# Performance work log

Measured on AMD Instinct MI355X. Metric: run time of the kernel, lower is better.

Reference implementation:

```python
import jax, jax.numpy as jnp
import numpy as np

N_NODES = 50000
N_EDGES = 1600000
N_HEAD = 4
F_OUT = 128


def setup_inputs() -> dict:
    key = jax.random.key(0)
    k1, k2, k3, k4 = jax.random.split(key, 4)
    x = jax.random.normal(k1, (N_NODES, F_OUT), dtype=jnp.float32)
    # diag weight [H,1,F]; small scale like xavier on a diag-ish param
    w = jax.random.normal(k2, (N_HEAD, 1, F_OUT), dtype=jnp.float32) * 0.1
    # a_src_dst init: uniform(-stdv, stdv), stdv = 1/sqrt(2*f_out)
    stdv = 1.0 / np.sqrt(2 * F_OUT)
    a = jax.random.uniform(k3, (N_HEAD, 2 * F_OUT, 1), dtype=jnp.float32, minval=-stdv, maxval=stdv)
    edge_index = jax.random.randint(k4, (2, N_EDGES), 0, N_NODES, dtype=jnp.int64)
    return {"x": x, "w": w, "a": a, "edge_index": edge_index}


def reference(x, w, a, edge_index):
    # x: [N,F], w: [H,1,F] (diag), a: [H,2F,1], edge_index: [2,E]
    H, F = w.shape[0], w.shape[-1]
    N = x.shape[0]
    src = edge_index[0]  # row indices (aggregation targets)
    dst = edge_index[1]
    h = x[None, :, :] * w  # [H,N,F]  (diag: elementwise scale per head)
    # split cat(h_src,h_dst)@a into two per-node projections (same math as concat+matmul)
    a_src = a[:, :F, 0]  # [H,F]
    a_dst = a[:, F:, 0]  # [H,F]
    s_src = jnp.einsum('hnf,hf->hn', h, a_src)  # [H,N]
    s_dst = jnp.einsum('hnf,hf->hn', h, a_dst)  # [H,N]
    score = s_src[:, src] + s_dst[:, dst]  # [H,E]
    edge_e = jnp.exp(-jax.nn.leaky_relu(score, negative_slope=0.2))  # [H,E]
    outs = []
    for i in range(H):  # small fixed head loop keeps peak memory at one head's messages
        rowsum = jax.ops.segment_sum(edge_e[i], src, num_segments=N)  # [N]
        msg = edge_e[i][:, None] * h[i][dst]  # [E,F]
        agg = jax.ops.segment_sum(msg, src, num_segments=N)  # [N,F]
        outs.append(agg / rowsum[:, None])
    return jnp.stack(outs, axis=0)  # [H,N,F]
```

## Files before the change

### kernel.cpp

```cpp
#include <hip/hip_runtime.h>

#define N_NODES 50000
#define N_EDGES 1600000
#define N_HEAD 4
#define F_OUT 128
#define CAP 96
#define NPS 512
#define K1 98
#define SCAP 17408
#define NPG 32
#define GROUPS 1563
#define EPB 4096
#define P1_BLOCKS ((N_EDGES + EPB - 1) / EPB)

__global__ void __launch_bounds__(256) score_kernel(
    const float* __restrict__ x, const float* __restrict__ w,
    const float* __restrict__ a, float4* __restrict__ s_src4,
    float4* __restrict__ s_dst4) {
  int wv = (blockIdx.x * blockDim.x + threadIdx.x) >> 6;
  int lane = threadIdx.x & 63;
  if (wv >= N_NODES) return;
  float xv0 = x[wv * F_OUT + lane];
  float xv1 = x[wv * F_OUT + 64 + lane];
  float ps[N_HEAD], pd[N_HEAD];
#pragma unroll
  for (int h = 0; h < N_HEAD; ++h) {
    float w0 = w[h * F_OUT + lane];
    float w1 = w[h * F_OUT + 64 + lane];
    float as0 = a[h * 2 * F_OUT + lane];
    float as1 = a[h * 2 * F_OUT + 64 + lane];
    float ad0 = a[h * 2 * F_OUT + F_OUT + lane];
    float ad1 = a[h * 2 * F_OUT + F_OUT + 64 + lane];
    ps[h] = xv0 * w0 * as0 + xv1 * w1 * as1;
    pd[h] = xv0 * w0 * ad0 + xv1 * w1 * ad1;
  }
#pragma unroll
  for (int off = 32; off > 0; off >>= 1) {
#pragma unroll
    for (int h = 0; h < N_HEAD; ++h) {
      ps[h] += __shfl_xor(ps[h], off, 64);
      pd[h] += __shfl_xor(pd[h], off, 64);
    }
  }
  if (lane == 0) {
    s_src4[wv] = make_float4(ps[0], ps[1], ps[2], ps[3]);
    s_dst4[wv] = make_float4(pd[0], pd[1], pd[2], pd[3]);
  }
}

__global__ void __launch_bounds__(256) partition_kernel(
    const int* __restrict__ src, const int* __restrict__ dst,
    int* __restrict__ gc, unsigned int* __restrict__ region) {
  __shared__ int hist[K1], cur[K1], lstart[K1], gpos[K1];
  __shared__ unsigned int staging[EPB];
  const int tid = threadIdx.x;
  const int base = blockIdx.x * EPB;
  int vc = N_EDGES - base;
  if (vc > EPB) vc = EPB;

  unsigned int pk[EPB / 256];
#pragma unroll
  for (int k = 0; k < EPB / 256; ++k) {
    int i = k * 256 + tid;
    if (i < vc) {
      unsigned int s = (unsigned int)src[base + i];
      unsigned int d = (unsigned int)dst[base + i];
      pk[k] = (s << 16) | d;
    } else {
      pk[k] = 0xffffffffu;
    }
  }
  if (tid < K1) { hist[tid] = 0; cur[tid] = 0; }
  __syncthreads();
#pragma unroll
  for (int k = 0; k < EPB / 256; ++k)
    if (pk[k] != 0xffffffffu) atomicAdd(&hist[pk[k] >> 25], 1);
  __syncthreads();
  if (tid < 64) {
    int carry = 0;
    for (int b0 = 0; b0 < K1; b0 += 64) {
      int idx = b0 + tid;
      int h = (idx < K1) ? hist[idx] : 0;
      int v = h;
#pragma unroll
      for (int off = 1; off < 64; off <<= 1) {
        int t = __shfl_up(v, off, 64);
        if (tid >= off) v += t;
      }
      if (idx < K1) {
        lstart[idx] = carry + v - h;
        gpos[idx] = atomicAdd(&gc[idx], h);
      }
      carry += __shfl(v, 63, 64);
    }
  }
  __syncthreads();
#pragma unroll
  for (int k = 0; k < EPB / 256; ++k) {
    if (pk[k] != 0xffffffffu) {
      int b = pk[k] >> 25;
      int pos = lstart[b] + atomicAdd(&cur[b], 1);
      staging[pos] = pk[k];
    }
  }
  __syncthreads();
  for (int i = tid; i < vc; i += 256) {
    unsigned int v = staging[i];
    int b = v >> 25;
    int off = gpos[b] + (i - lstart[b]);
    if (off < SCAP) region[(size_t)b * SCAP + off] = v;
  }
}

__global__ void __launch_bounds__(256) agg_kernel(
    const float* __restrict__ x, const float* __restrict__ w,
    const float4* __restrict__ s_src4, const float4* __restrict__ s_dst4,
    const int* __restrict__ gc, const unsigned int* __restrict__ region,
    float* __restrict__ out) {
  __shared__ int ncnt[NPG];
  __shared__ int nbkt[NPG][CAP];
  __shared__ float4 lds_w[4][CAP];
  const int tid = threadIdx.x;
  const int g = blockIdx.x;
  const int sb = g >> 4;
  int c = gc[sb];
  if (c > SCAP) c = SCAP;
  if (tid < NPG) ncnt[tid] = 0;
  __syncthreads();

  const unsigned int* reg = region + (size_t)sb * SCAP;
  const unsigned int gtag = (unsigned int)g;
  for (int i = tid; i < c; i += 256) {
    unsigned int v = reg[i];
    unsigned int s = v >> 16;
    if ((s >> 5) == gtag) {
      int l = s & 31;
      int p = atomicAdd(&ncnt[l], 1);
      if (p < CAP) nbkt[l][p] = (int)(v & 0xffffu);
    }
  }
  __syncthreads();

  const int ws = tid >> 6, lane = tid & 63;
  const float* xp = x + 2 * lane;

  for (int l = ws; l < NPG; l += 4) {
    int n = g * NPG + l;
    if (n >= N_NODES) break;
    int m = ncnt[l];
    m = (m < CAP) ? m : CAP;
    float4 ss = s_src4[n];

    float p0 = 0.f, p1 = 0.f, p2 = 0.f, p3 = 0.f;
    for (int j = lane; j < m; j += 64) {
      int d = nbkt[l][j];
      float4 sd = s_dst4[d];
      float sc0 = ss.x + sd.x, sc1 = ss.y + sd.y, sc2 = ss.z + sd.z, sc3 = ss.w + sd.w;
      float e0 = __expf(-fmaxf(sc0, 0.2f * sc0));
      float e1 = __expf(-fmaxf(sc1, 0.2f * sc1));
      float e2 = __expf(-fmaxf(sc2, 0.2f * sc2));
      float e3 = __expf(-fmaxf(sc3, 0.2f * sc3));
      lds_w[ws][j] = make_float4(e0, e1, e2, e3);
      p0 += e0; p1 += e1; p2 += e2; p3 += e3;
    }
#pragma unroll
    for (int off = 32; off > 0; off >>= 1) {
      p0 += __shfl_xor(p0, off, 64);
      p1 += __shfl_xor(p1, off, 64);
      p2 += __shfl_xor(p2, off, 64);
      p3 += __shfl_xor(p3, off, 64);
    }

    float2 a0 = {0.f, 0.f}, a1 = {0.f, 0.f}, a2 = {0.f, 0.f}, a3 = {0.f, 0.f};
    int j = 0;
    for (; j + 1 < m; j += 2) {
      int d0 = nbkt[l][j];
      int d1 = nbkt[l][j + 1];
      float4 w0 = lds_w[ws][j];
      float4 w1 = lds_w[ws][j + 1];
      float2 x0 = *(const float2*)(xp + (size_t)d0 * F_OUT);
      float2 x1 = *(const float2*)(xp + (size_t)d1 * F_OUT);
      a0.x = fmaf(w0.x, x0.x, a0.x); a0.y = fmaf(w0.x, x0.y, a0.y);
      a1.x = fmaf(w0.y, x0.x, a1.x); a1.y = fmaf(w0.y, x0.y, a1.y);
      a2.x = fmaf(w0.z, x0.x, a2.x); a2.y = fmaf(w0.z, x0.y, a2.y);
      a3.x = fmaf(w0.w, x0.x, a3.x); a3.y = fmaf(w0.w, x0.y, a3.y);
      a0.x = fmaf(w1.x, x1.x, a0.x); a0.y = fmaf(w1.x, x1.y, a0.y);
      a1.x = fmaf(w1.y, x1.x, a1.x); a1.y = fmaf(w1.y, x1.y, a1.y);
      a2.x = fmaf(w1.z, x1.x, a2.x); a2.y = fmaf(w1.z, x1.y, a2.y);
      a3.x = fmaf(w1.w, x1.x, a3.x); a3.y = fmaf(w1.w, x1.y, a3.y);
    }
    if (j < m) {
      int d0 = nbkt[l][j];
      float4 w0 = lds_w[ws][j];
      float2 x0 = *(const float2*)(xp + (size_t)d0 * F_OUT);
      a0.x = fmaf(w0.x, x0.x, a0.x); a0.y = fmaf(w0.x, x0.y, a0.y);
      a1.x = fmaf(w0.y, x0.x, a1.x); a1.y = fmaf(w0.y, x0.y, a1.y);
      a2.x = fmaf(w0.z, x0.x, a2.x); a2.y = fmaf(w0.z, x0.y, a2.y);
      a3.x = fmaf(w0.w, x0.x, a3.x); a3.y = fmaf(w0.w, x0.y, a3.y);
    }

    const float2 wl0 = *(const float2*)(w + 0 * F_OUT + 2 * lane);
    const float2 wl1 = *(const float2*)(w + 1 * F_OUT + 2 * lane);
    const float2 wl2 = *(const float2*)(w + 2 * F_OUT + 2 * lane);
    const float2 wl3 = *(const float2*)(w + 3 * F_OUT + 2 * lane);
    float r0 = 1.f / p0, r1 = 1.f / p1, r2 = 1.f / p2, r3 = 1.f / p3;

    float2 o;
    o.x = wl0.x * a0.x * r0; o.y = wl0.y * a0.y * r0;
    *(float2*)(out + ((size_t)0 * N_NODES + n) * F_OUT + 2 * lane) = o;
    o.x = wl1.x * a1.x * r1; o.y = wl1.y * a1.y * r1;
    *(float2*)(out + ((size_t)1 * N_NODES + n) * F_OUT + 2 * lane) = o;
    o.x = wl2.x * a2.x * r2; o.y = wl2.y * a2.y * r2;
    *(float2*)(out + ((size_t)2 * N_NODES + n) * F_OUT + 2 * lane) = o;
    o.x = wl3.x * a3.x * r3; o.y = wl3.y * a3.y * r3;
    *(float2*)(out + ((size_t)3 * N_NODES + n) * F_OUT + 2 * lane) = o;
  }
}

extern "C" void kernel_launch(void* const* d_in, const int* in_sizes, int n_in,
                              void* d_out, int out_size, void* d_ws, size_t ws_size,
                              hipStream_t stream) {
  const float* x = (const float*)d_in[0];
  const float* w = (const float*)d_in[1];
  const float* a = (const float*)d_in[2];
  const int* ei = (const int*)d_in[3];
  const int* src = ei;
  const int* dst = ei + N_EDGES;
  float* out = (float*)d_out;

  char* p = (char*)d_ws;
  float4* s_src4 = (float4*)p;      p += (size_t)N_NODES * 16;
  float4* s_dst4 = (float4*)p;      p += (size_t)N_NODES * 16;
  int* gc = (int*)p;                p += 4096;
  unsigned int* region = (unsigned int*)p;
  p += (size_t)K1 * SCAP * 4;

  hipMemsetAsync(gc, 0, 4096, stream);

  score_kernel<<<(N_NODES * 64 + 255) / 256, 256, 0, stream>>>(x, w, a, s_src4, s_dst4);
  partition_kernel<<<P1_BLOCKS, 256, 0, stream>>>(src, dst, gc, region);
  agg_kernel<<<GROUPS, 256, 0, stream>>>(x, w, s_src4, s_dst4, gc, region, out);
}
```

Baseline: 308.9 us.

## Use float4 half-wave gathers, smaller node groups, and fold memset into score kernel

```diff
diff --git a/kernel.cpp b/kernel.cpp
--- a/kernel.cpp
+++ b/kernel.cpp
@@ -8,15 +8,16 @@
 #define NPS 512
 #define K1 98
 #define SCAP 17408
-#define NPG 32
-#define GROUPS 1563
-#define EPB 4096
+#define NPG 16
+#define GROUPS 3125
+#define EPB 2048
 #define P1_BLOCKS ((N_EDGES + EPB - 1) / EPB)
 
 __global__ void __launch_bounds__(256) score_kernel(
     const float* __restrict__ x, const float* __restrict__ w,
     const float* __restrict__ a, float4* __restrict__ s_src4,
-    float4* __restrict__ s_dst4) {
+    float4* __restrict__ s_dst4, int* __restrict__ gc) {
+  if (blockIdx.x == 0 && threadIdx.x < K1) gc[threadIdx.x] = 0;
   int wv = (blockIdx.x * blockDim.x + threadIdx.x) >> 6;
   int lane = threadIdx.x & 63;
   if (wv >= N_NODES) return;
@@ -112,7 +113,7 @@
   }
 }
 
-__global__ void __launch_bounds__(256) agg_kernel(
+__global__ void __launch_bounds__(256, 8) agg_kernel(
     const float* __restrict__ x, const float* __restrict__ w,
     const float4* __restrict__ s_src4, const float4* __restrict__ s_dst4,
     const int* __restrict__ gc, const unsigned int* __restrict__ region,
@@ -122,7 +123,7 @@
   __shared__ float4 lds_w[4][CAP];
   const int tid = threadIdx.x;
   const int g = blockIdx.x;
-  const int sb = g >> 4;
+  const int sb = g >> 5;
   int c = gc[sb];
   if (c > SCAP) c = SCAP;
   if (tid < NPG) ncnt[tid] = 0;
@@ -133,8 +134,8 @@
   for (int i = tid; i < c; i += 256) {
     unsigned int v = reg[i];
     unsigned int s = v >> 16;
-    if ((s >> 5) == gtag) {
-      int l = s & 31;
+    if ((s >> 4) == gtag) {
+      int l = s & 15;
       int p = atomicAdd(&ncnt[l], 1);
       if (p < CAP) nbkt[l][p] = (int)(v & 0xffffu);
     }
@@ -142,7 +143,9 @@
   __syncthreads();
 
   const int ws = tid >> 6, lane = tid & 63;
-  const float* xp = x + 2 * lane;
+  const int half = lane >> 5, fl = lane & 31;
+  const float4* __restrict__ xq = (const float4*)x;
+  const float4* __restrict__ wq = (const float4*)w;
 
   for (int l = ws; l < NPG; l += 4) {
     int n = g * NPG + l;
@@ -171,49 +174,88 @@
       p3 += __shfl_xor(p3, off, 64);
     }
 
-    float2 a0 = {0.f, 0.f}, a1 = {0.f, 0.f}, a2 = {0.f, 0.f}, a3 = {0.f, 0.f};
+    float4 A0 = {0, 0, 0, 0}, A1 = {0, 0, 0, 0}, A2 = {0, 0, 0, 0}, A3 = {0, 0, 0, 0};
     int j = 0;
+    for (; j + 3 < m; j += 4) {
+      int da = nbkt[l][j + half];
+      int db = nbkt[l][j + 2 + half];
+      float4 wa = lds_w[ws][j + half];
+      float4 wb = lds_w[ws][j + 2 + half];
+      float4 xa = xq[(size_t)da * 32 + fl];
+      float4 xb = xq[(size_t)db * 32 + fl];
+      A0.x = fmaf(wa.x, xa.x, A0.x); A0.y = fmaf(wa.x, xa.y, A0.y);
+      A0.z = fmaf(wa.x, xa.z, A0.z); A0.w = fmaf(wa.x, xa.w, A0.w);
+      A1.x = fmaf(wa.y, xa.x, A1.x); A1.y = fmaf(wa.y, xa.y, A1.y);
+      A1.z = fmaf(wa.y, xa.z, A1.z); A1.w = fmaf(wa.y, xa.w, A1.w);
+      A2.x = fmaf(wa.z, xa.x, A2.x); A2.y = fmaf(wa.z, xa.y, A2.y);
+      A2.z = fmaf(wa.z, xa.z, A2.z); A2.w = fmaf(wa.z, xa.w, A2.w);
+      A3.x = fmaf(wa.w, xa.x, A3.x); A3.y = fmaf(wa.w, xa.y, A3.y);
+      A3.z = fmaf(wa.w, xa.z, A3.z); A3.w = fmaf(wa.w, xa.w, A3.w);
+      A0.x = fmaf(wb.x, xb.x, A0.x); A0.y = fmaf(wb.x, xb.y, A0.y);
+      A0.z = fmaf(wb.x, xb.z, A0.z); A0.w = fmaf(wb.x, xb.w, A0.w);
+      A1.x = fmaf(wb.y, xb.x, A1.x); A1.y = fmaf(wb.y, xb.y, A1.y);
+      A1.z = fmaf(wb.y, xb.z, A1.z); A1.w = fmaf(wb.y, xb.w, A1.w);
+      A2.x = fmaf(wb.z, xb.x, A2.x); A2.y = fmaf(wb.z, xb.y, A2.y);
+      A2.z = fmaf(wb.z, xb.z, A2.z); A2.w = fmaf(wb.z, xb.w, A2.w);
+      A3.x = fmaf(wb.w, xb.x, A3.x); A3.y = fmaf(wb.w, xb.y, A3.y);
+      A3.z = fmaf(wb.w, xb.z, A3.z); A3.w = fmaf(wb.w, xb.w, A3.w);
+    }
     for (; j + 1 < m; j += 2) {
-      int d0 = nbkt[l][j];
-      int d1 = nbkt[l][j + 1];
-      float4 w0 = lds_w[ws][j];
-      float4 w1 = lds_w[ws][j + 1];
-      float2 x0 = *(const float2*)(xp + (size_t)d0 * F_OUT);
-      float2 x1 = *(const float2*)(xp + (size_t)d1 * F_OUT);
-      a0.x = fmaf(w0.x, x0.x, a0.x); a0.y = fmaf(w0.x, x0.y, a0.y);
-      a1.x = fmaf(w0.y, x0.x, a1.x); a1.y = fmaf(w0.y, x0.y, a1.y);
-      a2.x = fmaf(w0.z, x0.x, a2.x); a2.y = fmaf(w0.z, x0.y, a2.y);
-      a3.x = fmaf(w0.w, x0.x, a3.x); a3.y = fmaf(w0.w, x0.y, a3.y);
-      a0.x = fmaf(w1.x, x1.x, a0.x); a0.y = fmaf(w1.x, x1.y, a0.y);
-      a1.x = fmaf(w1.y, x1.x, a1.x); a1.y = fmaf(w1.y, x1.y, a1.y);
-      a2.x = fmaf(w1.z, x1.x, a2.x); a2.y = fmaf(w1.z, x1.y, a2.y);
-      a3.x = fmaf(w1.w, x1.x, a3.x); a3.y = fmaf(w1.w, x1.y, a3.y);
+      int da = nbkt[l][j + half];
+      float4 wa = lds_w[ws][j + half];
+      float4 xa = xq[(size_t)da * 32 + fl];
+      A0.x = fmaf(wa.x, xa.x, A0.x); A0.y = fmaf(wa.x, xa.y, A0.y);
+      A0.z = fmaf(wa.x, xa.z, A0.z); A0.w = fmaf(wa.x, xa.w, A0.w);
+      A1.x = fmaf(wa.y, xa.x, A1.x); A1.y = fmaf(wa.y, xa.y, A1.y);
+      A1.z = fmaf(wa.y, xa.z, A1.z); A1.w = fmaf(wa.y, xa.w, A1.w);
+      A2.x = fmaf(wa.z, xa.x, A2.x); A2.y = fmaf(wa.z, xa.y, A2.y);
+      A2.z = fmaf(wa.z, xa.z, A2.z); A2.w = fmaf(wa.z, xa.w, A2.w);
+      A3.x = fmaf(wa.w, xa.x, A3.x); A3.y = fmaf(wa.w, xa.y, A3.y);
+      A3.z = fmaf(wa.w, xa.z, A3.z); A3.w = fmaf(wa.w, xa.w, A3.w);
     }
     if (j < m) {
-      int d0 = nbkt[l][j];
-      float4 w0 = lds_w[ws][j];
-      float2 x0 = *(const float2*)(xp + (size_t)d0 * F_OUT);
-      a0.x = fmaf(w0.x, x0.x, a0.x); a0.y = fmaf(w0.x, x0.y, a0.y);
-      a1.x = fmaf(w0.y, x0.x, a1.x); a1.y = fmaf(w0.y, x0.y, a1.y);
-      a2.x = fmaf(w0.z, x0.x, a2.x); a2.y = fmaf(w0.z, x0.y, a2.y);
-      a3.x = fmaf(w0.w, x0.x, a3.x); a3.y = fmaf(w0.w, x0.y, a3.y);
-    }
-
-    const float2 wl0 = *(const float2*)(w + 0 * F_OUT + 2 * lane);
-    const float2 wl1 = *(const float2*)(w + 1 * F_OUT + 2 * lane);
-    const float2 wl2 = *(const float2*)(w + 2 * F_OUT + 2 * lane);
-    const float2 wl3 = *(const float2*)(w + 3 * F_OUT + 2 * lane);
+      int da = nbkt[l][j];
+      float4 wa = lds_w[ws][j];
+      float4 xa = xq[(size_t)da * 32 + fl];
+      if (half == 0) {
+        A0.x = fmaf(wa.x, xa.x, A0.x); A0.y = fmaf(wa.x, xa.y, A0.y);
+        A0.z = fmaf(wa.x, xa.z, A0.z); A0.w = fmaf(wa.x, xa.w, A0.w);
+        A1.x = fmaf(wa.y, xa.x, A1.x); A1.y = fmaf(wa.y, xa.y, A1.y);
+        A1.z = fmaf(wa.y, xa.z, A1.z); A1.w = fmaf(wa.y, xa.w, A1.w);
+        A2.x = fmaf(wa.z, xa.x, A2.x); A2.y = fmaf(wa.z, xa.y, A2.y);
+        A2.z = fmaf(wa.z, xa.z, A2.z); A2.w = fmaf(wa.z, xa.w, A2.w);
+        A3.x = fmaf(wa.w, xa.x, A3.x); A3.y = fmaf(wa.w, xa.y, A3.y);
+        A3.z = fmaf(wa.w, xa.z, A3.z); A3.w = fmaf(wa.w, xa.w, A3.w);
+      }
+    }
+
+    A0.x += __shfl_xor(A0.x, 32, 64); A0.y += __shfl_xor(A0.y, 32, 64);
+    A0.z += __shfl_xor(A0.z, 32, 64); A0.w += __shfl_xor(A0.w, 32, 64);
+    A1.x += __shfl_xor(A1.x, 32, 64); A1.y += __shfl_xor(A1.y, 32, 64);
+    A1.z += __shfl_xor(A1.z, 32, 64); A1.w += __shfl_xor(A1.w, 32, 64);
+    A2.x += __shfl_xor(A2.x, 32, 64); A2.y += __shfl_xor(A2.y, 32, 64);
+    A2.z += __shfl_xor(A2.z, 32, 64); A2.w += __shfl_xor(A2.w, 32, 64);
+    A3.x += __shfl_xor(A3.x, 32, 64); A3.y += __shfl_xor(A3.y, 32, 64);
+    A3.z += __shfl_xor(A3.z, 32, 64); A3.w += __shfl_xor(A3.w, 32, 64);
+
     float r0 = 1.f / p0, r1 = 1.f / p1, r2 = 1.f / p2, r3 = 1.f / p3;
 
-    float2 o;
-    o.x = wl0.x * a0.x * r0; o.y = wl0.y * a0.y * r0;
-    *(float2*)(out + ((size_t)0 * N_NODES + n) * F_OUT + 2 * lane) = o;
-    o.x = wl1.x * a1.x * r1; o.y = wl1.y * a1.y * r1;
-    *(float2*)(out + ((size_t)1 * N_NODES + n) * F_OUT + 2 * lane) = o;
-    o.x = wl2.x * a2.x * r2; o.y = wl2.y * a2.y * r2;
-    *(float2*)(out + ((size_t)2 * N_NODES + n) * F_OUT + 2 * lane) = o;
-    o.x = wl3.x * a3.x * r3; o.y = wl3.y * a3.y * r3;
-    *(float2*)(out + ((size_t)3 * N_NODES + n) * F_OUT + 2 * lane) = o;
+    {
+      float4 acc; float rr; int h;
+      if (half == 0) { acc = A0; rr = r0; h = 0; } else { acc = A1; rr = r1; h = 1; }
+      float4 ww = wq[h * 32 + fl];
+      float4 o = {ww.x * acc.x * rr, ww.y * acc.y * rr,
+                  ww.z * acc.z * rr, ww.w * acc.w * rr};
+      ((float4*)out)[((size_t)h * N_NODES + n) * 32 + fl] = o;
+    }
+    {
+      float4 acc; float rr; int h;
+      if (half == 0) { acc = A2; rr = r2; h = 2; } else { acc = A3; rr = r3; h = 3; }
+      float4 ww = wq[h * 32 + fl];
+      float4 o = {ww.x * acc.x * rr, ww.y * acc.y * rr,
+                  ww.z * acc.z * rr, ww.w * acc.w * rr};
+      ((float4*)out)[((size_t)h * N_NODES + n) * 32 + fl] = o;
+    }
   }
 }
 
@@ -235,9 +277,7 @@
   unsigned int* region = (unsigned int*)p;
   p += (size_t)K1 * SCAP * 4;
 
-  hipMemsetAsync(gc, 0, 4096, stream);
-
-  score_kernel<<<(N_NODES * 64 + 255) / 256, 256, 0, stream>>>(x, w, a, s_src4, s_dst4);
+  score_kernel<<<(N_NODES * 64 + 255) / 256, 256, 0, stream>>>(x, w, a, s_src4, s_dst4, gc);
   partition_kernel<<<P1_BLOCKS, 256, 0, stream>>>(src, dst, gc, region);
   agg_kernel<<<GROUPS, 256, 0, stream>>>(x, w, s_src4, s_dst4, gc, region, out);
 }
```

New measurement: 333.1 us. +7.8%, slower.
